# Kernel tuning notes

Hardware: AMD Instinct MI355X
Metric: run time of the kernel (lower is better)

## Reference

```python
import jax, jax.numpy as jnp
import numpy as np

B, Himg, Wimg, C, HID, R = 16, 64, 64, 256, 512, 2
CLIP = 3.0
NULL_LOGIT = 0.0
WARMUP_ETA = 1.0


def _ln(x, g, b, eps=1e-5):
    m = x.mean(-1, keepdims=True)
    v = ((x - m) ** 2).mean(-1, keepdims=True)
    return (x - m) * jax.lax.rsqrt(v + eps) * g + b


def _mlp(x, W1, b1, W2, b2):
    # Linear -> GELU (erf, torch default) -> Linear
    return jax.nn.gelu(x @ W1 + b1, approximate=False) @ W2 + b2


def setup_inputs() -> dict:
    key = jax.random.key(0)
    ks = jax.random.split(key, 8)
    s = 0.02
    return {
        "states": jax.random.normal(ks[0], (B, Himg * Wimg, C), jnp.float32),
        "ln_c_g": jnp.ones((C,), jnp.float32),
        "ln_c_b": jnp.zeros((C,), jnp.float32),
        "parent_seed": jax.random.normal(ks[1], (1, 1, C), jnp.float32) * s,
        "dW1": jax.random.normal(ks[2], (3 * C, HID), jnp.float32) * s,
        "db1": jnp.zeros((HID,), jnp.float32),
        "dW2": jax.random.normal(ks[3], (HID, 1), jnp.float32) * s,
        "db2": jnp.zeros((1,), jnp.float32),
        "rW1": jax.random.normal(ks[4], (3 * C, HID), jnp.float32) * s,
        "rb1": jnp.zeros((HID,), jnp.float32),
        "rW2": jax.random.normal(ks[5], (HID, 1), jnp.float32) * s,
        "rb2": jnp.zeros((1,), jnp.float32),
        "vW": jax.random.normal(ks[6], (C, C), jnp.float32) * s,
        "vb": jnp.zeros((C,), jnp.float32),
        "e_bias": jnp.full((1,), -0.1, jnp.float32),
        "ln_o_g": jnp.ones((C,), jnp.float32),
        "ln_o_b": jnp.zeros((C,), jnp.float32),
        "image_h": Himg,
        "image_w": Wimg,
    }


def reference(states, ln_c_g, ln_c_b, parent_seed, dW1, db1, dW2, db2,
              rW1, rb1, rW2, rb2, vW, vb, e_bias, ln_o_g, ln_o_b,
              image_h, image_w):
    b = states.shape[0]
    ph, pw = image_h // R, image_w // R
    # [B,H,W,C] -> [B, ph*pw, R*R, C] local 2x2 child groups
    grid = states.reshape(b, image_h, image_w, C)
    groups = grid.reshape(b, ph, R, pw, R, C).transpose(0, 1, 3, 2, 4, 5)
    groups = groups.reshape(b, ph * pw, R * R, C)

    normalized = _ln(groups, ln_c_g, ln_c_b)            # child LayerNorm
    gm = normalized.mean(axis=2, keepdims=True)          # group mean (mask all-true)
    gm_b = jnp.broadcast_to(gm, normalized.shape)
    joint = jnp.concatenate([normalized, gm_b, normalized * gm_b], axis=-1)

    drive = _mlp(joint, dW1, db1, dW2, db2)              # [B,P,G,1]
    variance = ((normalized - gm) ** 2).mean(-1, keepdims=True)
    resistance = jax.nn.softplus(_mlp(joint, rW1, rb1, rW2, rb2)) + variance

    # EMLUnit: clipped drive/resistance energy with learned bias
    energy = jnp.clip(WARMUP_ETA * drive / (resistance + 1e-6) + e_bias,
                      -CLIP, CLIP)[..., 0]               # [B,P,G]

    # EMLResponsibility: null-aware softmax over children + null slot
    null = jnp.full(energy.shape[:-1] + (1,), NULL_LOGIT, energy.dtype)
    probs = jax.nn.softmax(jnp.concatenate([energy, null], axis=-1), axis=-1)
    weights = probs[..., :-1]                            # neighbor_weights [B,P,G]
    null_weight = probs[..., -1:]                        # [B,P,1]
    update_strength = 1.0 - null_weight                  # [B,P,1]

    values = normalized @ vW + vb                        # value_proj
    candidate = jnp.einsum('bpg,bpgc->bpc', weights, values)

    # EMLPrecisionUpdate with old_confidence=0: blend seed toward candidate
    old_state = parent_seed                              # broadcasts over [B,P,C]
    new_state = old_state + update_strength * (candidate - old_state)
    parent_state = _ln(new_state, ln_o_g, ln_o_b)
    return parent_state
```

## Files before the change

kernel.cpp:

```cpp
#include <hip/hip_runtime.h>
#include <hip/hip_bf16.h>
#include <math.h>

#define BATCH 16
#define PGRID 1024
#define NGRP  (BATCH*PGRID)
#define NELEM (NGRP*4)
#define CDIM  256
#define HID   512

#define OFF_NH    ((size_t)0)
#define OFF_NL    ((size_t)8388608)
#define OFF_GMH   ((size_t)16777216)
#define OFF_GML   ((size_t)18874368)
#define OFF_VAR   ((size_t)20971520)
#define OFF_DRIVE ((size_t)21037056)
#define OFF_RPRE  ((size_t)21102592)
#define OFF_WN    ((size_t)21168128)
#define OFF_US    ((size_t)25362432)
#define OFF_W1TH  ((size_t)25378816)
#define OFF_W1TL  ((size_t)25772032)

__device__ __forceinline__ unsigned short f2bf(float x) {
  unsigned u = __float_as_uint(x);
  unsigned r = u + 0x7FFFu + ((u >> 16) & 1u);
  return (unsigned short)(r >> 16);
}
__device__ __forceinline__ float bf2f(unsigned short h) {
  return __uint_as_float(((unsigned)h) << 16);
}

__device__ __forceinline__ void wave_reduce4(float v[4]) {
#pragma unroll
  for (int off = 1; off < 64; off <<= 1) {
#pragma unroll
    for (int i = 0; i < 4; ++i) v[i] += __shfl_xor(v[i], off, 64);
  }
}

__device__ __forceinline__ void block_reduce4(float v[4], float* sh ) {
  wave_reduce4(v);
  const int lane = threadIdx.x & 63, wid = threadIdx.x >> 6;
  __syncthreads();
  if (lane == 0) {
#pragma unroll
    for (int i = 0; i < 4; ++i) sh[wid * 4 + i] = v[i];
  }
  __syncthreads();
#pragma unroll
  for (int i = 0; i < 4; ++i) v[i] = sh[i] + sh[4 + i] + sh[8 + i] + sh[12 + i];
}

__global__ __launch_bounds__(256) void prep_kernel(
    const float* __restrict__ states,
    const float* __restrict__ ln_c_g, const float* __restrict__ ln_c_b,
    short* __restrict__ nh, short* __restrict__ nl,
    short* __restrict__ gmh, short* __restrict__ gml,
    float* __restrict__ varb, float* __restrict__ drive, float* __restrict__ rpre)
{
  __shared__ float sh[16];
  const int g = blockIdx.x;
  const int b = g >> 10;
  const int p = g & 1023;
  const int py = p >> 5, px = p & 31;
  const int c = threadIdx.x;

  float x[4];
#pragma unroll
  for (int s = 0; s < 4; ++s) {
    const int h = py * 2 + (s >> 1);
    const int w = px * 2 + (s & 1);
    x[s] = states[((size_t)(b * 4096 + h * 64 + w)) * CDIM + c];
  }

  float sum[4] = {x[0], x[1], x[2], x[3]};
  block_reduce4(sum, sh);
  float d[4];
#pragma unroll
  for (int s = 0; s < 4; ++s) d[s] = x[s] - sum[s] * (1.f / 256.f);

  float sq[4] = {d[0]*d[0], d[1]*d[1], d[2]*d[2], d[3]*d[3]};
  block_reduce4(sq, sh);

  const float gg = ln_c_g[c], bb = ln_c_b[c];
  float nn[4];
#pragma unroll
  for (int s = 0; s < 4; ++s)
    nn[s] = d[s] * rsqrtf(sq[s] * (1.f / 256.f) + 1e-5f) * gg + bb;

  const float gmc = 0.25f * (nn[0] + nn[1] + nn[2] + nn[3]);
  float e4[4];
#pragma unroll
  for (int s = 0; s < 4; ++s) { const float t = nn[s] - gmc; e4[s] = t * t; }
  block_reduce4(e4, sh);

  const size_t nb = (size_t)g * 4 * CDIM;
#pragma unroll
  for (int s = 0; s < 4; ++s) {
    const unsigned short h = f2bf(nn[s]);
    const unsigned short l = f2bf(nn[s] - bf2f(h));
    nh[nb + s * CDIM + c] = (short)h;
    nl[nb + s * CDIM + c] = (short)l;
  }
  {
    const unsigned short h = f2bf(gmc);
    const unsigned short l = f2bf(gmc - bf2f(h));
    gmh[(size_t)g * CDIM + c] = (short)h;
    gml[(size_t)g * CDIM + c] = (short)l;
  }
  if (c < 4) {
    varb[g * 4 + c] = e4[c] * (1.f / 256.f);
    drive[g * 4 + c] = 0.f;
    rpre[g * 4 + c] = 0.f;
  }
}

__global__ __launch_bounds__(256) void prew1_kernel(
    const float* __restrict__ dW1, const float* __restrict__ rW1,
    short* __restrict__ w1th, short* __restrict__ w1tl)
{
  const int col = blockIdx.x;
  const float* W1 = (col < 512) ? dW1 : rW1;
  const int cl = (col < 512) ? col : col - 512;
  for (int k = threadIdx.x; k < 768; k += 256) {
    const float x = W1[(size_t)k * HID + cl];
    const unsigned short h = f2bf(x);
    const unsigned short l = f2bf(x - bf2f(h));
    w1th[(size_t)col * 768 + k] = (short)h;
    w1tl[(size_t)col * 768 + k] = (short)l;
  }
}

typedef __attribute__((ext_vector_type(8))) short  frag_ab;
typedef __attribute__((ext_vector_type(4))) float  frag_cd;

#define AIDX(sec, row) ((sec) * 1024 + (row) * 8)

__global__ __launch_bounds__(256) void mlp_gemm_mfma(
    const short* __restrict__ nh, const short* __restrict__ nl,
    const short* __restrict__ gmh, const short* __restrict__ gml,
    const short* __restrict__ w1th, const short* __restrict__ w1tl,
    const float* __restrict__ db1, const float* __restrict__ rb1,
    const float* __restrict__ dW2, const float* __restrict__ rW2,
    float* __restrict__ drive, float* __restrict__ rpre)
{
  __shared__ __align__(16) short Ah[4096];
  __shared__ __align__(16) short Al[4096];
  __shared__ __align__(16) short Bh[4096];
  __shared__ __align__(16) short Bl[4096];

  const int tid  = threadIdx.x;
  const int lane = tid & 63;
  const int w    = tid >> 6;
  const int wm   = w >> 1;
  const int wn   = w & 1;

  const int bid = blockIdx.x;
  const int xcd = bid & 7;
  const int lb  = bid >> 3;
  const int mt  = xcd * 64 + (lb >> 3);
  const int nt  = lb & 7;
  const int m_base = mt * 128;
  const int n_base = nt * 128;

  const int ar = tid >> 1;
  const int ac = (tid & 1) * 16;
  const int asec = (tid & 1) * 2;
  const int e  = m_base + ar;
  const short* nhrow = nh + (size_t)e * CDIM;
  const short* nlrow = nl + (size_t)e * CDIM;
  const short* ghrow = gmh + (size_t)(e >> 2) * CDIM;
  const short* glrow = gml + (size_t)(e >> 2) * CDIM;

  const int bcol = tid >> 1;
  const int bk   = (tid & 1) * 16;
  const int bsec = (tid & 1) * 2;
  const short* bsrc_h = w1th + (size_t)(n_base + bcol) * 768 + bk;
  const short* bsrc_l = w1tl + (size_t)(n_base + bcol) * 768 + bk;

  frag_cd acc[4][4];
#pragma unroll
  for (int i = 0; i < 4; ++i)
#pragma unroll
    for (int j = 0; j < 4; ++j)
#pragma unroll
      for (int q = 0; q < 4; ++q) acc[i][j][q] = 0.f;

  frag_ab sA0, sA1, sA2, sA3;
  float va[16];
  frag_ab sB0, sB1, sB2, sB3;

#define LOADA(K0) {                                                          \
    if ((K0) < 256) {                                                        \
      sA0 = *(const frag_ab*)(nhrow + (K0) + ac);                            \
      sA1 = *(const frag_ab*)(nhrow + (K0) + ac + 8);                        \
      sA2 = *(const frag_ab*)(nlrow + (K0) + ac);                            \
      sA3 = *(const frag_ab*)(nlrow + (K0) + ac + 8);                        \
    } else if ((K0) < 512) {                                                 \
      const int kb_ = (K0) - 256;                                            \
      sA0 = *(const frag_ab*)(ghrow + kb_ + ac);                             \
      sA1 = *(const frag_ab*)(ghrow + kb_ + ac + 8);                         \
      sA2 = *(const frag_ab*)(glrow + kb_ + ac);                             \
      sA3 = *(const frag_ab*)(glrow + kb_ + ac + 8);                         \
    } else {                                                                 \
      const int kb_ = (K0) - 512;                                            \
      const frag_ab h0 = *(const frag_ab*)(nhrow + kb_ + ac);                \
      const frag_ab h1 = *(const frag_ab*)(nhrow + kb_ + ac + 8);            \
      const frag_ab l0 = *(const frag_ab*)(nlrow + kb_ + ac);                \
      const frag_ab l1 = *(const frag_ab*)(nlrow + kb_ + ac + 8);            \
      const frag_ab g0 = *(const frag_ab*)(ghrow + kb_ + ac);                \
      const frag_ab g1 = *(const frag_ab*)(ghrow + kb_ + ac + 8);            \
      const frag_ab m0 = *(const frag_ab*)(glrow + kb_ + ac);                \
      const frag_ab m1 = *(const frag_ab*)(glrow + kb_ + ac + 8);            \
      _Pragma("unroll")                                                      \
      for (int i_ = 0; i_ < 8; ++i_) {                                       \
        const float nf = bf2f((unsigned short)h0[i_]) + bf2f((unsigned short)l0[i_]); \
        const float gf = bf2f((unsigned short)g0[i_]) + bf2f((unsigned short)m0[i_]); \
        va[i_] = nf * gf;                                                    \
      }                                                                      \
      _Pragma("unroll")                                                      \
      for (int i_ = 0; i_ < 8; ++i_) {                                       \
        const float nf = bf2f((unsigned short)h1[i_]) + bf2f((unsigned short)l1[i_]); \
        const float gf = bf2f((unsigned short)g1[i_]) + bf2f((unsigned short)m1[i_]); \
        va[8 + i_] = nf * gf;                                                \
      }                                                                      \
    }                                                                        \
  }

#define LOADB(K0) {                                                          \
    sB0 = *(const frag_ab*)(bsrc_h + (K0));                                  \
    sB1 = *(const frag_ab*)(bsrc_h + (K0) + 8);                              \
    sB2 = *(const frag_ab*)(bsrc_l + (K0));                                  \
    sB3 = *(const frag_ab*)(bsrc_l + (K0) + 8);                              \
  }

  LOADA(0); LOADB(0);

  for (int kk = 0; kk < 24; ++kk) {
    __syncthreads();
    if (kk < 16) {
      *(frag_ab*)&Ah[AIDX(asec,     ar)] = sA0;
      *(frag_ab*)&Ah[AIDX(asec + 1, ar)] = sA1;
      *(frag_ab*)&Al[AIDX(asec,     ar)] = sA2;
      *(frag_ab*)&Al[AIDX(asec + 1, ar)] = sA3;
    } else {
      frag_ab ph0, ph1, pl0, pl1;
#pragma unroll
      for (int i = 0; i < 8; ++i) {
        const unsigned short h = f2bf(va[i]);
        ph0[i] = (short)h; pl0[i] = (short)f2bf(va[i] - bf2f(h));
      }
#pragma unroll
      for (int i = 0; i < 8; ++i) {
        const unsigned short h = f2bf(va[8 + i]);
        ph1[i] = (short)h; pl1[i] = (short)f2bf(va[8 + i] - bf2f(h));
      }
      *(frag_ab*)&Ah[AIDX(asec,     ar)] = ph0;
      *(frag_ab*)&Ah[AIDX(asec + 1, ar)] = ph1;
      *(frag_ab*)&Al[AIDX(asec,     ar)] = pl0;
      *(frag_ab*)&Al[AIDX(asec + 1, ar)] = pl1;
    }
    *(frag_ab*)&Bh[AIDX(bsec,     bcol)] = sB0;
    *(frag_ab*)&Bh[AIDX(bsec + 1, bcol)] = sB1;
    *(frag_ab*)&Bl[AIDX(bsec,     bcol)] = sB2;
    *(frag_ab*)&Bl[AIDX(bsec + 1, bcol)] = sB3;
    __syncthreads();

    if (kk < 23) { const int k0 = (kk + 1) * 32; LOADA(k0); LOADB(k0); }

    const int sec = lane >> 4;
    frag_ab bhf[4], blf[4];
#pragma unroll
    for (int nf = 0; nf < 4; ++nf) {
      const int cb = AIDX(sec, wn * 64 + nf * 16 + (lane & 15));
      bhf[nf] = *(const frag_ab*)&Bh[cb];
      blf[nf] = *(const frag_ab*)&Bl[cb];
    }
#pragma unroll
    for (int mf = 0; mf < 4; ++mf) {
      const int rb = AIDX(sec, wm * 64 + mf * 16 + (lane & 15));
      const frag_ab ahf = *(const frag_ab*)&Ah[rb];
      const frag_ab alf = *(const frag_ab*)&Al[rb];
#pragma unroll
      for (int nf = 0; nf < 4; ++nf) {
        acc[mf][nf] = __builtin_amdgcn_mfma_f32_16x16x32_bf16(ahf, bhf[nf], acc[mf][nf], 0, 0, 0);
        acc[mf][nf] = __builtin_amdgcn_mfma_f32_16x16x32_bf16(ahf, blf[nf], acc[mf][nf], 0, 0, 0);
        acc[mf][nf] = __builtin_amdgcn_mfma_f32_16x16x32_bf16(alf, bhf[nf], acc[mf][nf], 0, 0, 0);
      }
    }
  }

  const bool is_d = (n_base < 512);
  const float* b1v = is_d ? db1 : rb1;
  const float* W2v = is_d ? dW2 : rW2;
  float* tgt = is_d ? drive : rpre;
  const int joff = n_base - (is_d ? 0 : 512) + wn * 64;

  float part[4][4];
#pragma unroll
  for (int i = 0; i < 4; ++i)
#pragma unroll
    for (int q = 0; q < 4; ++q) part[i][q] = 0.f;

#pragma unroll
  for (int nf = 0; nf < 4; ++nf) {
    const int j = joff + nf * 16 + (lane & 15);
    const float bb = b1v[j];
    const float ww = W2v[j];
#pragma unroll
    for (int mf = 0; mf < 4; ++mf)
#pragma unroll
      for (int q = 0; q < 4; ++q) {
        const float xv = acc[mf][nf][q] + bb;
        const float ge = 0.5f * xv * (1.f + erff(xv * 0.70710678118654752f));
        part[mf][q] = fmaf(ge, ww, part[mf][q]);
      }
  }
#pragma unroll
  for (int off = 1; off < 16; off <<= 1)
#pragma unroll
    for (int mf = 0; mf < 4; ++mf)
#pragma unroll
      for (int q = 0; q < 4; ++q)
        part[mf][q] += __shfl_xor(part[mf][q], off, 64);

  if ((lane & 15) == 0) {
    const int rq = lane >> 4;
#pragma unroll
    for (int mf = 0; mf < 4; ++mf)
#pragma unroll
      for (int q = 0; q < 4; ++q)
        atomicAdd(&tgt[m_base + wm * 64 + mf * 16 + rq * 4 + q], part[mf][q]);
  }
}

__global__ __launch_bounds__(256) void weights_kernel(
    const short* __restrict__ nh, const short* __restrict__ nl,
    const float* __restrict__ drive, const float* __restrict__ rpre,
    const float* __restrict__ varb,
    const float* __restrict__ db2, const float* __restrict__ rb2,
    const float* __restrict__ e_bias,
    float* __restrict__ wn, float* __restrict__ usb)
{
  const int g = blockIdx.x;
  const int c = threadIdx.x;
  const float eb = e_bias[0];
  const float b2d = db2[0], b2r = rb2[0];

  float w[4];
  float mx = 0.f;
#pragma unroll
  for (int s = 0; s < 4; ++s) {
    const float dr = drive[g * 4 + s] + b2d;
    const float rp = rpre[g * 4 + s] + b2r;
    const float va = varb[g * 4 + s];
    const float sp = fmaxf(rp, 0.f) + log1pf(expf(-fabsf(rp)));
    float en = dr / (sp + va + 1e-6f) + eb;
    en = fminf(3.f, fmaxf(-3.f, en));
    w[s] = en;
    mx = fmaxf(mx, en);
  }
  const float nullw = expf(-mx);
  float Z = nullw;
#pragma unroll
  for (int s = 0; s < 4; ++s) { w[s] = expf(w[s] - mx); Z += w[s]; }
  const float inv = 1.f / Z;

  float a = 0.f;
  const size_t nb = (size_t)g * 4 * CDIM;
#pragma unroll
  for (int s = 0; s < 4; ++s) {
    const size_t ix = nb + s * CDIM + c;
    const float nv = bf2f((unsigned short)nh[ix]) + bf2f((unsigned short)nl[ix]);
    a = fmaf(w[s] * inv, nv, a);
  }
  wn[(size_t)g * CDIM + c] = a;
  if (c == 0) usb[g] = 1.f - nullw * inv;
}

__global__ __launch_bounds__(256) void final_kernel(
    const float* __restrict__ wn, const float* __restrict__ usb,
    const float* __restrict__ vW, const float* __restrict__ vb,
    const float* __restrict__ seed,
    const float* __restrict__ ln_o_g, const float* __restrict__ ln_o_b,
    float* __restrict__ out)
{
  __shared__ float lwn[16][256];
  const int t = threadIdx.x;
  const int g0 = blockIdx.x * 16;
#pragma unroll
  for (int gi = 0; gi < 16; ++gi)
    lwn[gi][t] = wn[(size_t)(g0 + gi) * CDIM + t];
  __syncthreads();

  const int cq = (t & 63) * 4;
  const int gq = (t >> 6) * 4;

  float acc[4][4];
#pragma unroll
  for (int gi = 0; gi < 4; ++gi)
#pragma unroll
    for (int j = 0; j < 4; ++j) acc[gi][j] = 0.f;

  for (int k = 0; k < 256; ++k) {
    const float4 w4 = *(const float4*)(vW + (size_t)k * CDIM + cq);
#pragma unroll
    for (int gi = 0; gi < 4; ++gi) {
      const float a = lwn[gq + gi][k];
      acc[gi][0] = fmaf(a, w4.x, acc[gi][0]);
      acc[gi][1] = fmaf(a, w4.y, acc[gi][1]);
      acc[gi][2] = fmaf(a, w4.z, acc[gi][2]);
      acc[gi][3] = fmaf(a, w4.w, acc[gi][3]);
    }
  }

  const float4 sd  = *(const float4*)(seed + cq);
  const float4 og  = *(const float4*)(ln_o_g + cq);
  const float4 ob  = *(const float4*)(ln_o_b + cq);
  const float4 vb4 = *(const float4*)(vb + cq);

#pragma unroll
  for (int gi = 0; gi < 4; ++gi) {
    const float us = usb[g0 + gq + gi];
    float nv[4];
    nv[0] = sd.x + us * (acc[gi][0] + us * vb4.x - sd.x);
    nv[1] = sd.y + us * (acc[gi][1] + us * vb4.y - sd.y);
    nv[2] = sd.z + us * (acc[gi][2] + us * vb4.z - sd.z);
    nv[3] = sd.w + us * (acc[gi][3] + us * vb4.w - sd.w);

    float s = nv[0] + nv[1] + nv[2] + nv[3];
#pragma unroll
    for (int off = 1; off < 64; off <<= 1) s += __shfl_xor(s, off, 64);
    const float m = s * (1.f / 256.f);

    const float d0 = nv[0] - m, d1 = nv[1] - m, d2 = nv[2] - m, d3 = nv[3] - m;
    float q = d0 * d0 + d1 * d1 + d2 * d2 + d3 * d3;
#pragma unroll
    for (int off = 1; off < 64; off <<= 1) q += __shfl_xor(q, off, 64);
    const float rstd = rsqrtf(q * (1.f / 256.f) + 1e-5f);

    float4 o;
    o.x = d0 * rstd * og.x + ob.x;
    o.y = d1 * rstd * og.y + ob.y;
    o.z = d2 * rstd * og.z + ob.z;
    o.w = d3 * rstd * og.w + ob.w;
    *(float4*)(out + (size_t)(g0 + gq + gi) * CDIM + cq) = o;
  }
}

extern "C" void kernel_launch(void* const* d_in, const int* in_sizes, int n_in,
                              void* d_out, int out_size, void* d_ws, size_t ws_size,
                              hipStream_t stream)
{
  const float* states = (const float*)d_in[0];
  const float* ln_c_g = (const float*)d_in[1];
  const float* ln_c_b = (const float*)d_in[2];
  const float* seed   = (const float*)d_in[3];
  const float* dW1    = (const float*)d_in[4];
  const float* db1    = (const float*)d_in[5];
  const float* dW2    = (const float*)d_in[6];
  const float* db2    = (const float*)d_in[7];
  const float* rW1    = (const float*)d_in[8];
  const float* rb1    = (const float*)d_in[9];
  const float* rW2    = (const float*)d_in[10];
  const float* rb2    = (const float*)d_in[11];
  const float* vW     = (const float*)d_in[12];
  const float* vb     = (const float*)d_in[13];
  const float* e_bias = (const float*)d_in[14];
  const float* ln_o_g = (const float*)d_in[15];
  const float* ln_o_b = (const float*)d_in[16];
  float* out = (float*)d_out;

  float* ws    = (float*)d_ws;
  short* nhb   = (short*)(ws + OFF_NH);
  short* nlb   = (short*)(ws + OFF_NL);
  short* gmhb  = (short*)(ws + OFF_GMH);
  short* gmlb  = (short*)(ws + OFF_GML);
  float* varb  = ws + OFF_VAR;
  float* drive = ws + OFF_DRIVE;
  float* rpre  = ws + OFF_RPRE;
  float* wnb   = ws + OFF_WN;
  float* usb   = ws + OFF_US;
  short* w1th  = (short*)(ws + OFF_W1TH);
  short* w1tl  = (short*)(ws + OFF_W1TL);

  prep_kernel<<<NGRP, 256, 0, stream>>>(states, ln_c_g, ln_c_b,
                                        nhb, nlb, gmhb, gmlb, varb, drive, rpre);

  prew1_kernel<<<1024, 256, 0, stream>>>(dW1, rW1, w1th, w1tl);

  mlp_gemm_mfma<<<4096, 256, 0, stream>>>(nhb, nlb, gmhb, gmlb, w1th, w1tl,
                                          db1, rb1, dW2, rW2, drive, rpre);

  weights_kernel<<<NGRP, 256, 0, stream>>>(nhb, nlb, drive, rpre, varb,
                                           db2, rb2, e_bias, wnb, usb);

  final_kernel<<<NGRP / 16, 256, 0, stream>>>(wnb, usb, vW, vb, seed,
                                              ln_o_g, ln_o_b, out);
}
```

Measured before the change: 842.9 us.

## Double-buffer LDS tiles in MLP GEMM to drop one barrier per k-step

The MFMA GEMM's shared-memory tiles become two ping-pong buffers. The next tile is written into the alternate buffer after the current tile's MFMAs, so each k-step needs one __syncthreads instead of two. The thread-to-row mapping for global loads is changed so each thread loads one row and a half-k slice. The gm*normalized product conversion is deferred to store time, which keeps 8 raw fragments live instead of 16 floats. LDS use doubles to 64 KB per block and launch_bounds requests 2 blocks per CU, which may limit occupancy or force register spills.

```diff
diff --git a/kernel.cpp b/kernel.cpp
--- a/kernel.cpp
+++ b/kernel.cpp
@@ -136,7 +136,7 @@
 
 #define AIDX(sec, row) ((sec) * 1024 + (row) * 8)
 
-__global__ __launch_bounds__(256) void mlp_gemm_mfma(
+__global__ __launch_bounds__(256, 2) void mlp_gemm_mfma(
     const short* __restrict__ nh, const short* __restrict__ nl,
     const short* __restrict__ gmh, const short* __restrict__ gml,
     const short* __restrict__ w1th, const short* __restrict__ w1tl,
@@ -144,10 +144,10 @@
     const float* __restrict__ dW2, const float* __restrict__ rW2,
     float* __restrict__ drive, float* __restrict__ rpre)
 {
-  __shared__ __align__(16) short Ah[4096];
-  __shared__ __align__(16) short Al[4096];
-  __shared__ __align__(16) short Bh[4096];
-  __shared__ __align__(16) short Bl[4096];
+  __shared__ __align__(16) short Ah[8192];
+  __shared__ __align__(16) short Al[8192];
+  __shared__ __align__(16) short Bh[8192];
+  __shared__ __align__(16) short Bl[8192];
 
   const int tid  = threadIdx.x;
   const int lane = tid & 63;
@@ -163,20 +163,17 @@
   const int m_base = mt * 128;
   const int n_base = nt * 128;
 
-  const int ar = tid >> 1;
-  const int ac = (tid & 1) * 16;
-  const int asec = (tid & 1) * 2;
-  const int e  = m_base + ar;
-  const short* nhrow = nh + (size_t)e * CDIM;
-  const short* nlrow = nl + (size_t)e * CDIM;
-  const short* ghrow = gmh + (size_t)(e >> 2) * CDIM;
-  const short* glrow = gml + (size_t)(e >> 2) * CDIM;
-
-  const int bcol = tid >> 1;
-  const int bk   = (tid & 1) * 16;
-  const int bsec = (tid & 1) * 2;
-  const short* bsrc_h = w1th + (size_t)(n_base + bcol) * 768 + bk;
-  const short* bsrc_l = w1tl + (size_t)(n_base + bcol) * 768 + bk;
+  const int srow = tid & 127;
+  const int sp   = tid >> 7;
+  const int sp16 = sp * 16;
+  const int sp2  = sp * 2;
+
+  const short* nhrow = nh  + (size_t)(m_base + srow) * CDIM;
+  const short* nlrow = nl  + (size_t)(m_base + srow) * CDIM;
+  const short* ghrow = gmh + (size_t)((m_base + srow) >> 2) * CDIM;
+  const short* glrow = gml + (size_t)((m_base + srow) >> 2) * CDIM;
+  const short* bsrc_h = w1th + (size_t)(n_base + srow) * 768 + sp16;
+  const short* bsrc_l = w1tl + (size_t)(n_base + srow) * 768 + sp16;
 
   frag_cd acc[4][4];
 #pragma unroll
@@ -186,99 +183,97 @@
 #pragma unroll
       for (int q = 0; q < 4; ++q) acc[i][j][q] = 0.f;
 
-  frag_ab sA0, sA1, sA2, sA3;
-  float va[16];
+  frag_ab rA0, rA1, rA2, rA3, rA4, rA5, rA6, rA7;
   frag_ab sB0, sB1, sB2, sB3;
 
-#define LOADA(K0) {                                                          \
-    if ((K0) < 256) {                                                        \
-      sA0 = *(const frag_ab*)(nhrow + (K0) + ac);                            \
-      sA1 = *(const frag_ab*)(nhrow + (K0) + ac + 8);                        \
-      sA2 = *(const frag_ab*)(nlrow + (K0) + ac);                            \
-      sA3 = *(const frag_ab*)(nlrow + (K0) + ac + 8);                        \
-    } else if ((K0) < 512) {                                                 \
-      const int kb_ = (K0) - 256;                                            \
-      sA0 = *(const frag_ab*)(ghrow + kb_ + ac);                             \
-      sA1 = *(const frag_ab*)(ghrow + kb_ + ac + 8);                         \
-      sA2 = *(const frag_ab*)(glrow + kb_ + ac);                             \
-      sA3 = *(const frag_ab*)(glrow + kb_ + ac + 8);                         \
-    } else {                                                                 \
-      const int kb_ = (K0) - 512;                                            \
-      const frag_ab h0 = *(const frag_ab*)(nhrow + kb_ + ac);                \
-      const frag_ab h1 = *(const frag_ab*)(nhrow + kb_ + ac + 8);            \
-      const frag_ab l0 = *(const frag_ab*)(nlrow + kb_ + ac);                \
-      const frag_ab l1 = *(const frag_ab*)(nlrow + kb_ + ac + 8);            \
-      const frag_ab g0 = *(const frag_ab*)(ghrow + kb_ + ac);                \
-      const frag_ab g1 = *(const frag_ab*)(ghrow + kb_ + ac + 8);            \
-      const frag_ab m0 = *(const frag_ab*)(glrow + kb_ + ac);                \
-      const frag_ab m1 = *(const frag_ab*)(glrow + kb_ + ac + 8);            \
-      _Pragma("unroll")                                                      \
-      for (int i_ = 0; i_ < 8; ++i_) {                                       \
-        const float nf = bf2f((unsigned short)h0[i_]) + bf2f((unsigned short)l0[i_]); \
-        const float gf = bf2f((unsigned short)g0[i_]) + bf2f((unsigned short)m0[i_]); \
-        va[i_] = nf * gf;                                                    \
-      }                                                                      \
-      _Pragma("unroll")                                                      \
-      for (int i_ = 0; i_ < 8; ++i_) {                                       \
-        const float nf = bf2f((unsigned short)h1[i_]) + bf2f((unsigned short)l1[i_]); \
-        const float gf = bf2f((unsigned short)g1[i_]) + bf2f((unsigned short)m1[i_]); \
-        va[8 + i_] = nf * gf;                                                \
-      }                                                                      \
-    }                                                                        \
-  }
-
-#define LOADB(K0) {                                                          \
-    sB0 = *(const frag_ab*)(bsrc_h + (K0));                                  \
-    sB1 = *(const frag_ab*)(bsrc_h + (K0) + 8);                              \
-    sB2 = *(const frag_ab*)(bsrc_l + (K0));                                  \
-    sB3 = *(const frag_ab*)(bsrc_l + (K0) + 8);                              \
-  }
+#define LOADA(K0) do {                                                   \
+    const int k0_ = (K0);                                                \
+    if (k0_ < 256) {                                                     \
+      const short* p_ = nhrow + k0_ + sp16;                              \
+      const short* q_ = nlrow + k0_ + sp16;                              \
+      rA0 = *(const frag_ab*)(p_);  rA1 = *(const frag_ab*)(p_ + 8);     \
+      rA2 = *(const frag_ab*)(q_);  rA3 = *(const frag_ab*)(q_ + 8);     \
+    } else if (k0_ < 512) {                                              \
+      const short* p_ = ghrow + (k0_ - 256) + sp16;                      \
+      const short* q_ = glrow + (k0_ - 256) + sp16;                      \
+      rA0 = *(const frag_ab*)(p_);  rA1 = *(const frag_ab*)(p_ + 8);     \
+      rA2 = *(const frag_ab*)(q_);  rA3 = *(const frag_ab*)(q_ + 8);     \
+    } else {                                                             \
+      const int kb_ = k0_ - 512;                                         \
+      const short* p_ = nhrow + kb_ + sp16;                              \
+      const short* q_ = nlrow + kb_ + sp16;                              \
+      const short* r_ = ghrow + kb_ + sp16;                              \
+      const short* s_ = glrow + kb_ + sp16;                              \
+      rA0 = *(const frag_ab*)(p_);  rA1 = *(const frag_ab*)(p_ + 8);     \
+      rA2 = *(const frag_ab*)(q_);  rA3 = *(const frag_ab*)(q_ + 8);     \
+      rA4 = *(const frag_ab*)(r_);  rA5 = *(const frag_ab*)(r_ + 8);     \
+      rA6 = *(const frag_ab*)(s_);  rA7 = *(const frag_ab*)(s_ + 8);     \
+    }                                                                    \
+  } while (0)
+
+#define LOADB(K0) do {                                                   \
+    sB0 = *(const frag_ab*)(bsrc_h + (K0));                              \
+    sB1 = *(const frag_ab*)(bsrc_h + (K0) + 8);                          \
+    sB2 = *(const frag_ab*)(bsrc_l + (K0));                              \
+    sB3 = *(const frag_ab*)(bsrc_l + (K0) + 8);                          \
+  } while (0)
+
+#define STOREAB(BUF, RAW) do {                                           \
+    const int bo_ = (BUF) * 4096;                                        \
+    if (RAW) {                                                           \
+      *(frag_ab*)&Ah[bo_ + AIDX(sp2,     srow)] = rA0;                   \
+      *(frag_ab*)&Ah[bo_ + AIDX(sp2 + 1, srow)] = rA1;                   \
+      *(frag_ab*)&Al[bo_ + AIDX(sp2,     srow)] = rA2;                   \
+      *(frag_ab*)&Al[bo_ + AIDX(sp2 + 1, srow)] = rA3;                   \
+    } else {                                                             \
+      frag_ab ph0, ph1, pl0, pl1;                                        \
+      _Pragma("unroll")                                                  \
+      for (int j_ = 0; j_ < 8; ++j_) {                                   \
+        const float n0 = bf2f((unsigned short)rA0[j_]) + bf2f((unsigned short)rA2[j_]); \
+        const float g0 = bf2f((unsigned short)rA4[j_]) + bf2f((unsigned short)rA6[j_]); \
+        const float p0 = n0 * g0;                                        \
+        const unsigned short h0_ = f2bf(p0);                             \
+        ph0[j_] = (short)h0_; pl0[j_] = (short)f2bf(p0 - bf2f(h0_));     \
+        const float n1 = bf2f((unsigned short)rA1[j_]) + bf2f((unsigned short)rA3[j_]); \
+        const float g1 = bf2f((unsigned short)rA5[j_]) + bf2f((unsigned short)rA7[j_]); \
+        const float p1 = n1 * g1;                                        \
+        const unsigned short h1_ = f2bf(p1);                             \
+        ph1[j_] = (short)h1_; pl1[j_] = (short)f2bf(p1 - bf2f(h1_));     \
+      }                                                                  \
+      *(frag_ab*)&Ah[bo_ + AIDX(sp2,     srow)] = ph0;                   \
+      *(frag_ab*)&Ah[bo_ + AIDX(sp2 + 1, srow)] = ph1;                   \
+      *(frag_ab*)&Al[bo_ + AIDX(sp2,     srow)] = pl0;                   \
+      *(frag_ab*)&Al[bo_ + AIDX(sp2 + 1, srow)] = pl1;                   \
+    }                                                                    \
+    *(frag_ab*)&Bh[bo_ + AIDX(sp2,     srow)] = sB0;                     \
+    *(frag_ab*)&Bh[bo_ + AIDX(sp2 + 1, srow)] = sB1;                     \
+    *(frag_ab*)&Bl[bo_ + AIDX(sp2,     srow)] = sB2;                     \
+    *(frag_ab*)&Bl[bo_ + AIDX(sp2 + 1, srow)] = sB3;                     \
+  } while (0)
 
   LOADA(0); LOADB(0);
+  STOREAB(0, true);
+  __syncthreads();
+  int cur = 0;
+
+  const int l15 = lane & 15;
+  const int sec = lane >> 4;
 
   for (int kk = 0; kk < 24; ++kk) {
-    __syncthreads();
-    if (kk < 16) {
-      *(frag_ab*)&Ah[AIDX(asec,     ar)] = sA0;
-      *(frag_ab*)&Ah[AIDX(asec + 1, ar)] = sA1;
-      *(frag_ab*)&Al[AIDX(asec,     ar)] = sA2;
-      *(frag_ab*)&Al[AIDX(asec + 1, ar)] = sA3;
-    } else {
-      frag_ab ph0, ph1, pl0, pl1;
-#pragma unroll
-      for (int i = 0; i < 8; ++i) {
-        const unsigned short h = f2bf(va[i]);
-        ph0[i] = (short)h; pl0[i] = (short)f2bf(va[i] - bf2f(h));
-      }
-#pragma unroll
-      for (int i = 0; i < 8; ++i) {
-        const unsigned short h = f2bf(va[8 + i]);
-        ph1[i] = (short)h; pl1[i] = (short)f2bf(va[8 + i] - bf2f(h));
-      }
-      *(frag_ab*)&Ah[AIDX(asec,     ar)] = ph0;
-      *(frag_ab*)&Ah[AIDX(asec + 1, ar)] = ph1;
-      *(frag_ab*)&Al[AIDX(asec,     ar)] = pl0;
-      *(frag_ab*)&Al[AIDX(asec + 1, ar)] = pl1;
-    }
-    *(frag_ab*)&Bh[AIDX(bsec,     bcol)] = sB0;
-    *(frag_ab*)&Bh[AIDX(bsec + 1, bcol)] = sB1;
-    *(frag_ab*)&Bl[AIDX(bsec,     bcol)] = sB2;
-    *(frag_ab*)&Bl[AIDX(bsec + 1, bcol)] = sB3;
-    __syncthreads();
-
-    if (kk < 23) { const int k0 = (kk + 1) * 32; LOADA(k0); LOADB(k0); }
-
-    const int sec = lane >> 4;
+    const bool havenext = (kk < 23);
+    if (havenext) { const int k0 = (kk + 1) * 32; LOADA(k0); LOADB(k0); }
+
+    const int bo = cur * 4096;
     frag_ab bhf[4], blf[4];
 #pragma unroll
     for (int nf = 0; nf < 4; ++nf) {
-      const int cb = AIDX(sec, wn * 64 + nf * 16 + (lane & 15));
+      const int cb = bo + AIDX(sec, wn * 64 + nf * 16 + l15);
       bhf[nf] = *(const frag_ab*)&Bh[cb];
       blf[nf] = *(const frag_ab*)&Bl[cb];
     }
 #pragma unroll
     for (int mf = 0; mf < 4; ++mf) {
-      const int rb = AIDX(sec, wm * 64 + mf * 16 + (lane & 15));
+      const int rb = bo + AIDX(sec, wm * 64 + mf * 16 + l15);
       const frag_ab ahf = *(const frag_ab*)&Ah[rb];
       const frag_ab alf = *(const frag_ab*)&Al[rb];
 #pragma unroll
@@ -288,6 +283,12 @@
         acc[mf][nf] = __builtin_amdgcn_mfma_f32_16x16x32_bf16(alf, bhf[nf], acc[mf][nf], 0, 0, 0);
       }
     }
+
+    if (havenext) {
+      STOREAB(cur ^ 1, (kk + 1) < 16);
+      __syncthreads();
+      cur ^= 1;
+    }
   }
 
   const bool is_d = (n_base < 512);
@@ -304,7 +305,7 @@
 
 #pragma unroll
   for (int nf = 0; nf < 4; ++nf) {
-    const int j = joff + nf * 16 + (lane & 15);
+    const int j = joff + nf * 16 + l15;
     const float bb = b1v[j];
     const float ww = W2v[j];
 #pragma unroll
@@ -324,7 +325,7 @@
       for (int q = 0; q < 4; ++q)
         part[mf][q] += __shfl_xor(part[mf][q], off, 64);
 
-  if ((lane & 15) == 0) {
+  if (l15 == 0) {
     const int rq = lane >> 4;
 #pragma unroll
     for (int mf = 0; mf < 4; ++mf)
```

Measured after the change: 722.3 us. 14.3% less time.
